# Optimization experiments

Measured on AMD Instinct MI355X. Metric: run time of the kernel, lower is better.

The kernel has to match this reference:

```python
import jax, jax.numpy as jnp
import numpy as np

NEG_INF = -1e15  # matches masked_fill value -1000000000000000.0
ALPHA = 0.2      # leakyReLU negative slope


def setup_inputs() -> dict:
    key = jax.random.key(0)
    k1, k2, k3, k4 = jax.random.split(key, 4)
    N, F_IN, F_OUT = 8192, 256, 64
    x = jax.random.normal(k1, (N, F_IN), dtype=jnp.float32)
    mask = jax.random.randint(k2, (N, N), 0, 2, dtype=jnp.int32)
    trans = jax.random.normal(k3, (F_IN, F_OUT), dtype=jnp.float32) * 0.1
    attn = jax.random.normal(k4, (2 * F_OUT, 1), dtype=jnp.float32) * 0.1
    return {"x": x, "mask": mask, "trans": trans, "attn": attn}


def reference(x, mask, trans, attn):
    d = trans.shape[1]
    h = x @ trans                                  # [N, d]
    e1 = h @ attn[:d, :]                           # [N, 1]
    e2 = h @ attn[d:, :]                           # [N, 1]
    scores = jax.nn.leaky_relu(e1 + e2.T, negative_slope=ALPHA)  # [N, N]
    masked = jnp.where(mask == 0, NEG_INF, scores)
    attention = jax.nn.softmax(masked, axis=1)
    return attention @ h                           # [N, d]
```

## Files before the change

kernel.cpp:

```cpp
#include <hip/hip_runtime.h>
#include <hip/hip_bf16.h>
#include <math.h>

#define N 8192
#define FIN 256
#define D 64
#define ALPHA 0.2f
#define SROW 1040
#define WBUF (16 * SROW)
#define CS 2048

typedef __attribute__((ext_vector_type(8))) short bf16x8;
typedef __attribute__((ext_vector_type(4))) float f32x4;

__global__ __launch_bounds__(256) void k_h_e(
    const float* __restrict__ x, const float* __restrict__ trans,
    const float* __restrict__ attn,
    __hip_bfloat16* __restrict__ hF, float* __restrict__ e1, float* __restrict__ e2)
{
    __shared__ float xs[8 * FIN];
    __shared__ __hip_bfloat16 hl[8 * D];
    const int t = threadIdx.x;
    const int r0 = blockIdx.x * 8;

    #pragma unroll
    for (int v = 0; v < 2; ++v) {
        int idx = t + 256 * v;
        ((float4*)xs)[idx] = ((const float4*)(x + (size_t)r0 * FIN))[idx];
    }
    __syncthreads();

    const int lane = t & 63, w = t >> 6;
    const float* xa = xs + (2 * w) * FIN;
    const float* xb = xs + (2 * w + 1) * FIN;
    float acca = 0.f, accb = 0.f;
    #pragma unroll 8
    for (int k = 0; k < FIN; ++k) {
        const float tv = trans[k * D + lane];
        acca = fmaf(xa[k], tv, acca);
        accb = fmaf(xb[k], tv, accb);
    }
    const int ra = r0 + 2 * w, rb = ra + 1;

    const float a1 = attn[lane], a2 = attn[D + lane];
    float p1a = acca * a1, p2a = acca * a2;
    float p1b = accb * a1, p2b = accb * a2;
    #pragma unroll
    for (int mm = 1; mm <= 32; mm <<= 1) {
        p1a += __shfl_xor(p1a, mm);
        p2a += __shfl_xor(p2a, mm);
        p1b += __shfl_xor(p1b, mm);
        p2b += __shfl_xor(p2b, mm);
    }
    if (lane == 0) { e1[ra] = p1a; e2[ra] = p2a; e1[rb] = p1b; e2[rb] = p2b; }

    hl[(2 * w) * D + lane]     = __float2bfloat16(acca);
    hl[(2 * w + 1) * D + lane] = __float2bfloat16(accb);
    __syncthreads();
    if (t < D) {
        const int q = t >> 4, m = t & 15;
        const int cb = r0 >> 5, jgrp = (r0 >> 3) & 3;
        union { bf16x8 v; __hip_bfloat16 h[8]; } o;
        #pragma unroll
        for (int r = 0; r < 8; ++r) o.h[r] = hl[r * D + q * 16 + m];
        *(bf16x8*)(hF + (((size_t)cb * 4 + q) * 64 + jgrp * 16 + m) * 8) = o.v;
    }
}

__global__ __launch_bounds__(256) void k_attn(
    const int* __restrict__ mask, const __hip_bfloat16* __restrict__ hF,
    const float* __restrict__ e1, const float* __restrict__ e2,
    float* __restrict__ out)
{
    __shared__ __align__(16) char smem[4 * WBUF];
    __shared__ float lw[4][16];
    const int t = threadIdx.x;
    const int lane = t & 63, wave = t >> 6;
    const int i0 = blockIdx.x * 16;
    const int c0 = wave * CS;
    const int m = lane & 15, quad = lane >> 4;
    const int row = i0 + m;
    const float er = e1[row];

    char* sw = smem + wave * WBUF;
    const char* swm = sw + m * SROW;
    const __hip_bfloat16* hfp = hF + (((size_t)(c0 >> 5)) * 4 * 64 + lane) * 8;

    f32x4 acc0 = {0.f, 0.f, 0.f, 0.f};
    f32x4 acc1 = {0.f, 0.f, 0.f, 0.f};
    f32x4 acc2 = {0.f, 0.f, 0.f, 0.f};
    f32x4 acc3 = {0.f, 0.f, 0.f, 0.f};
    float lsum = 0.f;

    const int nss = CS >> 8;

    for (int ss = 0; ss < nss; ++ss) {
        const int cb0 = c0 + ss * 256;
        #pragma unroll
        for (int r = 0; r < 16; ++r) {
            const int* g = mask + (size_t)(i0 + r) * N + cb0 + lane * 4;
            char* l = sw + r * SROW + lane * 16;
            __builtin_amdgcn_global_load_lds(
                (const __attribute__((address_space(1))) void*)g,
                (__attribute__((address_space(3))) void*)l, 16, 0, 2 );
        }
        __builtin_amdgcn_s_waitcnt(0x0F70);

        const int itg0 = ss * 8;
        bf16x8 pb0, pb1, pb2, pb3; float4 pea, peb;
        {
            const size_t ito = (size_t)itg0 * 2048;
            pb0 = *(const bf16x8*)(hfp + ito);
            pb1 = *(const bf16x8*)(hfp + ito + 512);
            pb2 = *(const bf16x8*)(hfp + ito + 1024);
            pb3 = *(const bf16x8*)(hfp + ito + 1536);
            const int jb = cb0 + quad * 8;
            pea = *(const float4*)(e2 + jb);
            peb = *(const float4*)(e2 + jb + 4);
        }
        #pragma unroll
        for (int p = 0; p < 8; ++p) {
            const bf16x8 b0 = pb0, b1 = pb1, b2 = pb2, b3 = pb3;
            const float4 ea = pea, eb = peb;
            if (p < 7) {
                const size_t ito = (size_t)(itg0 + p + 1) * 2048;
                pb0 = *(const bf16x8*)(hfp + ito);
                pb1 = *(const bf16x8*)(hfp + ito + 512);
                pb2 = *(const bf16x8*)(hfp + ito + 1024);
                pb3 = *(const bf16x8*)(hfp + ito + 1536);
                const int jb = cb0 + (p + 1) * 32 + quad * 8;
                pea = *(const float4*)(e2 + jb);
                peb = *(const float4*)(e2 + jb + 4);
            }
            const int4 m0 = *(const int4*)(swm + p * 128 + quad * 32);
            const int4 m1 = *(const int4*)(swm + p * 128 + quad * 32 + 16);

            float s0 = er + ea.x; s0 = s0 > 0.f ? s0 : ALPHA * s0;
            float s1 = er + ea.y; s1 = s1 > 0.f ? s1 : ALPHA * s1;
            float s2 = er + ea.z; s2 = s2 > 0.f ? s2 : ALPHA * s2;
            float s3 = er + ea.w; s3 = s3 > 0.f ? s3 : ALPHA * s3;
            float s4 = er + eb.x; s4 = s4 > 0.f ? s4 : ALPHA * s4;
            float s5 = er + eb.y; s5 = s5 > 0.f ? s5 : ALPHA * s5;
            float s6 = er + eb.z; s6 = s6 > 0.f ? s6 : ALPHA * s6;
            float s7 = er + eb.w; s7 = s7 > 0.f ? s7 : ALPHA * s7;
            const float p0 = m0.x ? __expf(s0) : 0.f;
            const float p1 = m0.y ? __expf(s1) : 0.f;
            const float p2 = m0.z ? __expf(s2) : 0.f;
            const float p3 = m0.w ? __expf(s3) : 0.f;
            const float p4 = m1.x ? __expf(s4) : 0.f;
            const float p5 = m1.y ? __expf(s5) : 0.f;
            const float p6 = m1.z ? __expf(s6) : 0.f;
            const float p7 = m1.w ? __expf(s7) : 0.f;

            union { bf16x8 v; __hip_bfloat162 h2[4]; } af;
            af.h2[0] = __float22bfloat162_rn(make_float2(p0, p1));
            af.h2[1] = __float22bfloat162_rn(make_float2(p2, p3));
            af.h2[2] = __float22bfloat162_rn(make_float2(p4, p5));
            af.h2[3] = __float22bfloat162_rn(make_float2(p6, p7));

            lsum += ((p0 + p1) + (p2 + p3)) + ((p4 + p5) + (p6 + p7));

            acc0 = __builtin_amdgcn_mfma_f32_16x16x32_bf16(af.v, b0, acc0, 0, 0, 0);
            acc1 = __builtin_amdgcn_mfma_f32_16x16x32_bf16(af.v, b1, acc1, 0, 0, 0);
            acc2 = __builtin_amdgcn_mfma_f32_16x16x32_bf16(af.v, b2, acc2, 0, 0, 0);
            acc3 = __builtin_amdgcn_mfma_f32_16x16x32_bf16(af.v, b3, acc3, 0, 0, 0);
        }
    }

    lsum += __shfl_xor(lsum, 16);
    lsum += __shfl_xor(lsum, 32);
    if (quad == 0) lw[wave][m] = lsum;

    __syncthreads();
    float* cw = (float*)smem;
    #pragma unroll
    for (int reg = 0; reg < 4; ++reg) {
        float* rbase = cw + (wave * 16 + quad * 4 + reg) * 64;
        rbase[m     ] = acc0[reg];
        rbase[m + 16] = acc1[reg];
        rbase[m + 32] = acc2[reg];
        rbase[m + 48] = acc3[reg];
    }
    __syncthreads();
    #pragma unroll
    for (int rr = 0; rr < 4; ++rr) {
        const int idx = rr * 256 + t;
        const int r = idx >> 6, c = idx & 63;
        float s = ((cw[(0 * 16 + r) * 64 + c] + cw[(1 * 16 + r) * 64 + c])
                +   cw[(2 * 16 + r) * 64 + c]) + cw[(3 * 16 + r) * 64 + c];
        float l = ((lw[0][r] + lw[1][r]) + lw[2][r]) + lw[3][r];
        out[(size_t)(i0 + r) * D + c] = s / l;
    }
}

extern "C" void kernel_launch(void* const* d_in, const int* in_sizes, int n_in,
                              void* d_out, int out_size, void* d_ws, size_t ws_size,
                              hipStream_t stream) {
    const float* x     = (const float*)d_in[0];
    const int*   mask  = (const int*)d_in[1];
    const float* trans = (const float*)d_in[2];
    const float* attn  = (const float*)d_in[3];
    float* out = (float*)d_out;

    char* ws = (char*)d_ws;
    __hip_bfloat16* hF = (__hip_bfloat16*)ws;
    char* p = ws + (size_t)D * N * sizeof(__hip_bfloat16);
    float* e1 = (float*)p;            p += (size_t)N * sizeof(float);
    float* e2 = (float*)p;            p += (size_t)N * sizeof(float);

    k_h_e<<<N / 8, 256, 0, stream>>>(x, trans, attn, hF, e1, e2);
    k_attn<<<N / 16, 256, 0, stream>>>(mask, hF, e1, e2, out);
}
```

Measured before the change: 382.8 us.

## Fuse projection and attention kernels with a grid-wide atomic barrier

Merges the h/e projection kernel into the attention kernel. Each of 512 blocks computes 16 rows of h, e1 and e2, then signals an atomic counter and spins until every block has arrived before reading the shared hF and e2. While waiting, the first mask tile is already issued into LDS, so the projection and barrier overlap with the mask load. This removes one kernel launch and the gap between kernels, at the cost of a hipMemsetAsync and a spin barrier that needs all 512 blocks resident at once, which could deadlock if occupancy is too low.

```diff
diff --git a/kernel.cpp b/kernel.cpp
--- a/kernel.cpp
+++ b/kernel.cpp
@@ -9,80 +9,100 @@
 #define SROW 1040
 #define WBUF (16 * SROW)
 #define CS 2048
+#define NBLK 512
 
 typedef __attribute__((ext_vector_type(8))) short bf16x8;
 typedef __attribute__((ext_vector_type(4))) float f32x4;
 
-__global__ __launch_bounds__(256) void k_h_e(
-    const float* __restrict__ x, const float* __restrict__ trans,
-    const float* __restrict__ attn,
-    __hip_bfloat16* __restrict__ hF, float* __restrict__ e1, float* __restrict__ e2)
-{
-    __shared__ float xs[8 * FIN];
-    __shared__ __hip_bfloat16 hl[8 * D];
-    const int t = threadIdx.x;
-    const int r0 = blockIdx.x * 8;
-
-    #pragma unroll
-    for (int v = 0; v < 2; ++v) {
-        int idx = t + 256 * v;
-        ((float4*)xs)[idx] = ((const float4*)(x + (size_t)r0 * FIN))[idx];
-    }
-    __syncthreads();
-
-    const int lane = t & 63, w = t >> 6;
-    const float* xa = xs + (2 * w) * FIN;
-    const float* xb = xs + (2 * w + 1) * FIN;
-    float acca = 0.f, accb = 0.f;
-    #pragma unroll 8
-    for (int k = 0; k < FIN; ++k) {
-        const float tv = trans[k * D + lane];
-        acca = fmaf(xa[k], tv, acca);
-        accb = fmaf(xb[k], tv, accb);
-    }
-    const int ra = r0 + 2 * w, rb = ra + 1;
-
-    const float a1 = attn[lane], a2 = attn[D + lane];
-    float p1a = acca * a1, p2a = acca * a2;
-    float p1b = accb * a1, p2b = accb * a2;
-    #pragma unroll
-    for (int mm = 1; mm <= 32; mm <<= 1) {
-        p1a += __shfl_xor(p1a, mm);
-        p2a += __shfl_xor(p2a, mm);
-        p1b += __shfl_xor(p1b, mm);
-        p2b += __shfl_xor(p2b, mm);
-    }
-    if (lane == 0) { e1[ra] = p1a; e2[ra] = p2a; e1[rb] = p1b; e2[rb] = p2b; }
-
-    hl[(2 * w) * D + lane]     = __float2bfloat16(acca);
-    hl[(2 * w + 1) * D + lane] = __float2bfloat16(accb);
-    __syncthreads();
-    if (t < D) {
-        const int q = t >> 4, m = t & 15;
-        const int cb = r0 >> 5, jgrp = (r0 >> 3) & 3;
-        union { bf16x8 v; __hip_bfloat16 h[8]; } o;
-        #pragma unroll
-        for (int r = 0; r < 8; ++r) o.h[r] = hl[r * D + q * 16 + m];
-        *(bf16x8*)(hF + (((size_t)cb * 4 + q) * 64 + jgrp * 16 + m) * 8) = o.v;
-    }
-}
-
-__global__ __launch_bounds__(256) void k_attn(
-    const int* __restrict__ mask, const __hip_bfloat16* __restrict__ hF,
-    const float* __restrict__ e1, const float* __restrict__ e2,
-    float* __restrict__ out)
+__global__ __launch_bounds__(256, 4) void k_fused(
+    const float* __restrict__ x, const int* __restrict__ mask,
+    const float* __restrict__ trans, const float* __restrict__ attn,
+    __hip_bfloat16* __restrict__ hF, float* __restrict__ e1,
+    float* __restrict__ e2, float* __restrict__ out,
+    unsigned* __restrict__ flag)
 {
     __shared__ __align__(16) char smem[4 * WBUF];
     __shared__ float lw[4][16];
     const int t = threadIdx.x;
+    const int b = blockIdx.x;
     const int lane = t & 63, wave = t >> 6;
-    const int i0 = blockIdx.x * 16;
+
+    {
+        float* xs = (float*)smem;
+        __hip_bfloat16* hl = (__hip_bfloat16*)(smem + 16 * FIN * 4);
+        const int r0 = b * 16;
+
+        #pragma unroll
+        for (int v = 0; v < 4; ++v) {
+            int idx = t + 256 * v;
+            ((float4*)xs)[idx] = ((const float4*)(x + (size_t)r0 * FIN))[idx];
+        }
+        __syncthreads();
+
+        float acc[4] = {0.f, 0.f, 0.f, 0.f};
+        const float* xr = xs + (4 * wave) * FIN;
+        #pragma unroll 4
+        for (int k = 0; k < FIN; ++k) {
+            const float tv = trans[k * D + lane];
+            acc[0] = fmaf(xr[k], tv, acc[0]);
+            acc[1] = fmaf(xr[k + FIN], tv, acc[1]);
+            acc[2] = fmaf(xr[k + 2 * FIN], tv, acc[2]);
+            acc[3] = fmaf(xr[k + 3 * FIN], tv, acc[3]);
+        }
+
+        const float a1 = attn[lane], a2 = attn[D + lane];
+        #pragma unroll
+        for (int j = 0; j < 4; ++j) {
+            float p1 = acc[j] * a1, p2 = acc[j] * a2;
+            #pragma unroll
+            for (int mm = 1; mm <= 32; mm <<= 1) {
+                p1 += __shfl_xor(p1, mm);
+                p2 += __shfl_xor(p2, mm);
+            }
+            if (lane == 0) { e1[r0 + 4 * wave + j] = p1; e2[r0 + 4 * wave + j] = p2; }
+            hl[(4 * wave + j) * D + lane] = __float2bfloat16(acc[j]);
+        }
+        __syncthreads();
+        if (t < 128) {
+            const int half = t >> 6, tt = t & 63;
+            const int q = tt >> 4, m = tt & 15;
+            const int rg0 = r0 + 8 * half;
+            const int cb = rg0 >> 5, jgrp = (rg0 >> 3) & 3;
+            union { bf16x8 v; __hip_bfloat16 h[8]; } o;
+            #pragma unroll
+            for (int r = 0; r < 8; ++r) o.h[r] = hl[(8 * half + r) * D + q * 16 + m];
+            *(bf16x8*)(hF + (((size_t)cb * 4 + q) * 64 + jgrp * 16 + m) * 8) = o.v;
+        }
+        __syncthreads();
+    }
+
+    const int i0 = b * 16;
     const int c0 = wave * CS;
+    char* sw = smem + wave * WBUF;
+
+    __threadfence();
+    if (t == 0)
+        __hip_atomic_fetch_add(flag, 1u, __ATOMIC_ACQ_REL, __HIP_MEMORY_SCOPE_AGENT);
+
+    #pragma unroll
+    for (int r = 0; r < 16; ++r) {
+        const int* g = mask + (size_t)(i0 + r) * N + c0 + lane * 4;
+        char* l = sw + r * SROW + lane * 16;
+        __builtin_amdgcn_global_load_lds(
+            (const __attribute__((address_space(1))) void*)g,
+            (__attribute__((address_space(3))) void*)l, 16, 0, 2 );
+    }
+
+    if (t == 0) {
+        while (__hip_atomic_load(flag, __ATOMIC_ACQUIRE, __HIP_MEMORY_SCOPE_AGENT)
+               < (unsigned)NBLK) { }
+    }
+    __syncthreads();
+    __threadfence();
+
     const int m = lane & 15, quad = lane >> 4;
     const int row = i0 + m;
     const float er = e1[row];
-
-    char* sw = smem + wave * WBUF;
     const char* swm = sw + m * SROW;
     const __hip_bfloat16* hfp = hF + (((size_t)(c0 >> 5)) * 4 * 64 + lane) * 8;
 
@@ -96,13 +116,15 @@
 
     for (int ss = 0; ss < nss; ++ss) {
         const int cb0 = c0 + ss * 256;
-        #pragma unroll
-        for (int r = 0; r < 16; ++r) {
-            const int* g = mask + (size_t)(i0 + r) * N + cb0 + lane * 4;
-            char* l = sw + r * SROW + lane * 16;
-            __builtin_amdgcn_global_load_lds(
-                (const __attribute__((address_space(1))) void*)g,
-                (__attribute__((address_space(3))) void*)l, 16, 0, 2 );
+        if (ss > 0) {
+            #pragma unroll
+            for (int r = 0; r < 16; ++r) {
+                const int* g = mask + (size_t)(i0 + r) * N + cb0 + lane * 4;
+                char* l = sw + r * SROW + lane * 16;
+                __builtin_amdgcn_global_load_lds(
+                    (const __attribute__((address_space(1))) void*)g,
+                    (__attribute__((address_space(3))) void*)l, 16, 0, 2 );
+            }
         }
         __builtin_amdgcn_s_waitcnt(0x0F70);
 
@@ -207,7 +229,8 @@
     char* p = ws + (size_t)D * N * sizeof(__hip_bfloat16);
     float* e1 = (float*)p;            p += (size_t)N * sizeof(float);
     float* e2 = (float*)p;            p += (size_t)N * sizeof(float);
-
-    k_h_e<<<N / 8, 256, 0, stream>>>(x, trans, attn, hF, e1, e2);
-    k_attn<<<N / 16, 256, 0, stream>>>(mask, hF, e1, e2, out);
+    unsigned* flag = (unsigned*)p;
+
+    hipMemsetAsync(flag, 0, sizeof(unsigned), stream);
+    k_fused<<<NBLK, 256, 0, stream>>>(x, mask, trans, attn, hF, e1, e2, out, flag);
 }
```

Result: slower. 489.1 us (+27.8%).

## Split attention columns across two blocks per row tile and add reduce kernel

Applied to the files above, without the earlier changes.

The column range of each 16-row tile is split across two blocks on a 2D grid, so twice as many blocks run. Each wave's mask staging buffer shrinks to 128 columns, loaded with two 4-byte global_load_lds per row instead of one 16-byte load. That halves LDS per block, and launch bounds now ask for 4 blocks per CU. Partial accumulators and row sums go to workspace, and a new reduce kernel combines them and divides. The aim is more resident waves to hide mask-load latency, at the cost of extra partial-result traffic, a third launch and narrower per-lane loads.

```diff
diff --git a/kernel.cpp b/kernel.cpp
--- a/kernel.cpp
+++ b/kernel.cpp
@@ -6,9 +6,10 @@
 #define FIN 256
 #define D 64
 #define ALPHA 0.2f
-#define SROW 1040
+#define SROW 528
 #define WBUF (16 * SROW)
-#define CS 2048
+#define NSPLIT 2
+#define CS 1024
 
 typedef __attribute__((ext_vector_type(8))) short bf16x8;
 typedef __attribute__((ext_vector_type(4))) float f32x4;
@@ -67,17 +68,18 @@
     }
 }
 
-__global__ __launch_bounds__(256) void k_attn(
+__global__ __launch_bounds__(256, 4) void k_attn(
     const int* __restrict__ mask, const __hip_bfloat16* __restrict__ hF,
     const float* __restrict__ e1, const float* __restrict__ e2,
-    float* __restrict__ out)
+    float* __restrict__ acc_part, float* __restrict__ l_part)
 {
     __shared__ __align__(16) char smem[4 * WBUF];
     __shared__ float lw[4][16];
     const int t = threadIdx.x;
     const int lane = t & 63, wave = t >> 6;
-    const int i0 = blockIdx.x * 16;
-    const int c0 = wave * CS;
+    const int sp = blockIdx.x;
+    const int i0 = blockIdx.y * 16;
+    const int c0 = sp * (NSPLIT == 2 ? 4096 : 0) + wave * CS;
     const int m = lane & 15, quad = lane >> 4;
     const int row = i0 + m;
     const float er = e1[row];
@@ -92,21 +94,24 @@
     f32x4 acc3 = {0.f, 0.f, 0.f, 0.f};
     float lsum = 0.f;
 
-    const int nss = CS >> 8;
+    const int nss = CS >> 7;
 
     for (int ss = 0; ss < nss; ++ss) {
-        const int cb0 = c0 + ss * 256;
+        const int cb0 = c0 + ss * 128;
         #pragma unroll
         for (int r = 0; r < 16; ++r) {
-            const int* g = mask + (size_t)(i0 + r) * N + cb0 + lane * 4;
-            char* l = sw + r * SROW + lane * 16;
+            const int* g = mask + (size_t)(i0 + r) * N + cb0 + lane;
+            char* l = sw + r * SROW + lane * 4;
             __builtin_amdgcn_global_load_lds(
                 (const __attribute__((address_space(1))) void*)g,
-                (__attribute__((address_space(3))) void*)l, 16, 0, 2 );
+                (__attribute__((address_space(3))) void*)l, 4, 0, 2 );
+            __builtin_amdgcn_global_load_lds(
+                (const __attribute__((address_space(1))) void*)(g + 64),
+                (__attribute__((address_space(3))) void*)(l + 256), 4, 0, 2);
         }
         __builtin_amdgcn_s_waitcnt(0x0F70);
 
-        const int itg0 = ss * 8;
+        const int itg0 = ss * 4;
         bf16x8 pb0, pb1, pb2, pb3; float4 pea, peb;
         {
             const size_t ito = (size_t)itg0 * 2048;
@@ -119,10 +124,10 @@
             peb = *(const float4*)(e2 + jb + 4);
         }
         #pragma unroll
-        for (int p = 0; p < 8; ++p) {
+        for (int p = 0; p < 4; ++p) {
             const bf16x8 b0 = pb0, b1 = pb1, b2 = pb2, b3 = pb3;
             const float4 ea = pea, eb = peb;
-            if (p < 7) {
+            if (p < 3) {
                 const size_t ito = (size_t)(itg0 + p + 1) * 2048;
                 pb0 = *(const bf16x8*)(hfp + ito);
                 pb1 = *(const bf16x8*)(hfp + ito + 512);
@@ -188,9 +193,23 @@
         const int r = idx >> 6, c = idx & 63;
         float s = ((cw[(0 * 16 + r) * 64 + c] + cw[(1 * 16 + r) * 64 + c])
                 +   cw[(2 * 16 + r) * 64 + c]) + cw[(3 * 16 + r) * 64 + c];
-        float l = ((lw[0][r] + lw[1][r]) + lw[2][r]) + lw[3][r];
-        out[(size_t)(i0 + r) * D + c] = s / l;
-    }
+        acc_part[((size_t)sp * N + i0 + r) * D + c] = s;
+        if (idx < 64 && (idx & 3) == 0) {  }
+    }
+    if (t < 16)
+        l_part[(size_t)sp * N + i0 + t]
+            = ((lw[0][t] + lw[1][t]) + lw[2][t]) + lw[3][t];
+}
+
+__global__ __launch_bounds__(256) void k_reduce(
+    const float* __restrict__ acc_part, const float* __restrict__ l_part,
+    float* __restrict__ out)
+{
+    const int idx = blockIdx.x * 256 + threadIdx.x;
+    const int row = idx >> 6;
+    float sum = acc_part[idx] + acc_part[(size_t)N * D + idx];
+    float l = l_part[row] + l_part[(size_t)N + row];
+    out[idx] = sum / l;
 }
 
 extern "C" void kernel_launch(void* const* d_in, const int* in_sizes, int n_in,
@@ -207,7 +226,11 @@
     char* p = ws + (size_t)D * N * sizeof(__hip_bfloat16);
     float* e1 = (float*)p;            p += (size_t)N * sizeof(float);
     float* e2 = (float*)p;            p += (size_t)N * sizeof(float);
+    float* l_part = (float*)p;        p += (size_t)NSPLIT * N * sizeof(float);
+    float* acc_part = (float*)p;
 
     k_h_e<<<N / 8, 256, 0, stream>>>(x, trans, attn, hF, e1, e2);
-    k_attn<<<N / 16, 256, 0, stream>>>(mask, hF, e1, e2, out);
-}
+    dim3 g2(NSPLIT, N / 16);
+    k_attn<<<g2, 256, 0, stream>>>(mask, hF, e1, e2, acc_part, l_part);
+    k_reduce<<<(N * D) / 256, 256, 0, stream>>>(acc_part, l_part, out);
+}
```

Result: no change. 383.7 us (+0.2%).
